# Performance work log

Hardware: AMD Instinct MI355X
Metric: run time of the kernel (lower is better)

## Reference

```python
import jax, jax.numpy as jnp
import numpy as np

# OPT-1.3B attention, decode phase with paged KV cache
E = 2048      # embed_dim
H = 32        # num_heads
D = E // H    # head_dim = 64
S = 64        # num decoding sequences (q_len = 1 each)
L = 2048      # max context length per sequence
BS = 16       # cache block size (vLLM default)
BPS = L // BS # blocks per sequence = 128
NB = S * BPS  # total cache blocks = 8192


def setup_inputs() -> dict:
    key = jax.random.key(0)
    ks = jax.random.split(key, 6)
    hidden_states = jax.random.normal(ks[0], (S, E), jnp.float32) * 0.02
    wqkv = jax.random.normal(ks[1], (E, 3 * E), jnp.float32) * 0.02
    bqkv = jnp.zeros((3 * E,), jnp.float32)
    wout = jax.random.normal(ks[2], (E, E), jnp.float32) * 0.02
    bout = jnp.zeros((E,), jnp.float32)
    key_cache = jax.random.normal(ks[3], (NB, BS, H, D), jnp.float32)
    value_cache = jax.random.normal(ks[4], (NB, BS, H, D), jnp.float32)
    # each sequence owns BPS distinct cache blocks (non-contiguous in general)
    block_tables = jnp.arange(S * BPS, dtype=jnp.int32).reshape(S, BPS)
    context_lens = jax.random.randint(ks[5], (S,), L // 2, L + 1).astype(jnp.int32)
    return dict(hidden_states=hidden_states, wqkv=wqkv, bqkv=bqkv,
                wout=wout, bout=bout, key_cache=key_cache,
                value_cache=value_cache, block_tables=block_tables,
                context_lens=context_lens)


def reference(hidden_states, wqkv, bqkv, wout, bout,
              key_cache, value_cache, block_tables, context_lens):
    scale = 1.0 / np.sqrt(D).astype(np.float32)
    # fused QKV projection
    qkv = hidden_states @ wqkv + bqkv                    # [S, 3E]
    q, k, v = jnp.split(qkv, 3, axis=-1)
    q = q.reshape(S, H, D)
    k_new = k.reshape(S, 1, H, D)
    v_new = v.reshape(S, 1, H, D)
    # paged gather of the KV cache: [S, BPS, BS, H, D] -> [S, L, H, D]
    keys = key_cache[block_tables].reshape(S, L, H, D)
    vals = value_cache[block_tables].reshape(S, L, H, D)
    # decode step attends over cached context plus the current token
    keys = jnp.concatenate([keys, k_new], axis=1)        # [S, L+1, H, D]
    vals = jnp.concatenate([vals, v_new], axis=1)
    scores = jnp.einsum('shd,slhd->shl', q, keys) * scale
    pos = jnp.arange(L + 1)
    valid = (pos[None, :] < context_lens[:, None]) | (pos[None, :] == L)
    scores = jnp.where(valid[:, None, :], scores, jnp.float32(-1e30))
    probs = jax.nn.softmax(scores, axis=-1)              # [S, H, L+1]
    attn = jnp.einsum('shl,slhd->shd', probs, vals).reshape(S, E)
    # output projection
    return attn @ wout + bout
```

## Files before the change

kernel.cpp:

```cpp
#include <hip/hip_runtime.h>
#include <math.h>

#define S_ 64
#define E_ 2048
#define H_ 32
#define D_ 64
#define L_ 2048
#define BS_ 16
#define BPS_ 128
#define QKV_N (3 * E_)
#define CHUNK_CB 8
#define MAXCH 16

__global__ __launch_bounds__(256) void gemm_part(const float* __restrict__ A,
                                                 const float* __restrict__ B,
                                                 float* __restrict__ P,
                                                 int K, int N) {
    __shared__ float As[64][32];
    const int t    = threadIdx.x;
    const int lane = t & 63;
    const int mg   = t >> 6;
    const int colbase = blockIdx.x * 128 + lane * 2;
    const int kchunk  = K / gridDim.y;
    const int ks      = blockIdx.y * kchunk;

    float2 acc[16];
#pragma unroll
    for (int mm = 0; mm < 16; ++mm) acc[mm] = make_float2(0.f, 0.f);

    for (int k0 = ks; k0 < ks + kchunk; k0 += 32) {
        __syncthreads();
#pragma unroll
        for (int i = 0; i < 2; ++i) {
            int f4  = t + i * 256;
            int row = f4 >> 3, c4 = f4 & 7;
            *(float4*)&As[row][c4 * 4] =
                *(const float4*)(A + (size_t)row * K + k0 + c4 * 4);
        }
        __syncthreads();
#pragma unroll
        for (int kk = 0; kk < 32; kk += 4) {
            float2 b0 = *(const float2*)(B + (size_t)(k0 + kk + 0) * N + colbase);
            float2 b1 = *(const float2*)(B + (size_t)(k0 + kk + 1) * N + colbase);
            float2 b2 = *(const float2*)(B + (size_t)(k0 + kk + 2) * N + colbase);
            float2 b3 = *(const float2*)(B + (size_t)(k0 + kk + 3) * N + colbase);
#pragma unroll
            for (int mm = 0; mm < 16; ++mm) {
                float4 a = *(const float4*)&As[mg * 16 + mm][kk];
                acc[mm].x = fmaf(a.x, b0.x, acc[mm].x);
                acc[mm].y = fmaf(a.x, b0.y, acc[mm].y);
                acc[mm].x = fmaf(a.y, b1.x, acc[mm].x);
                acc[mm].y = fmaf(a.y, b1.y, acc[mm].y);
                acc[mm].x = fmaf(a.z, b2.x, acc[mm].x);
                acc[mm].y = fmaf(a.z, b2.y, acc[mm].y);
                acc[mm].x = fmaf(a.w, b3.x, acc[mm].x);
                acc[mm].y = fmaf(a.w, b3.y, acc[mm].y);
            }
        }
    }
    float* Pb = P + (size_t)blockIdx.y * 64 * N;
#pragma unroll
    for (int mm = 0; mm < 16; ++mm)
        *(float2*)(Pb + (size_t)(mg * 16 + mm) * N + colbase) = acc[mm];
}

__global__ __launch_bounds__(256) void reduce_add(const float* __restrict__ P,
                                                  const float* __restrict__ bias,
                                                  float* __restrict__ C,
                                                  int N, int nparts) {
    const int i4     = blockIdx.x * 256 + threadIdx.x;
    const int total4 = 64 * N / 4;
    const int col4   = i4 % (N / 4);
    float4 s = ((const float4*)bias)[col4];
    for (int k = 0; k < nparts; ++k) {
        float4 p = ((const float4*)P)[(size_t)k * total4 + i4];
        s.x += p.x; s.y += p.y; s.z += p.z; s.w += p.w;
    }
    ((float4*)C)[i4] = s;
}

__global__ __launch_bounds__(256, 6) void attn_row(
        const float* __restrict__ qkv,
        const float* __restrict__ kcache,
        const float* __restrict__ vcache,
        const int* __restrict__ btab,
        const int* __restrict__ clens,
        float* __restrict__ ml,
        float* __restrict__ pacc) {
    const int s   = blockIdx.x >> 4;
    const int c   = blockIdx.x & 15;
    const int ctx = clens[s];
    const int nb  = (ctx + 15) >> 4;
    const int cb0 = c * CHUNK_CB;
    if (cb0 >= nb) return;
    const int cb1 = min(cb0 + CHUNK_CB, nb);
    const int t   = threadIdx.x;

    const float* qb = qkv + (size_t)s * QKV_N;
    const float4 q0 = *(const float4*)(qb + t * 4);
    const float4 q1 = *(const float4*)(qb + 1024 + t * 4);

    float m0 = -1e30f, l0 = 0.f, m1 = -1e30f, l1 = 0.f;
    float4 a0 = make_float4(0.f, 0.f, 0.f, 0.f);
    float4 a1 = make_float4(0.f, 0.f, 0.f, 0.f);

    const int* bt = btab + s * BPS_;
    for (int cb = cb0; cb < cb1; ++cb) {
        const int blk = bt[cb];
        const float* kb = kcache + (size_t)blk * (BS_ * H_ * D_);
        const float* vb = vcache + (size_t)blk * (BS_ * H_ * D_);
#pragma unroll 2
        for (int i = 0; i < 16; ++i) {
            const int   tok = cb * 16 + i;
            const int   off = i * 2048 + t * 4;
            const float4 k0 = *(const float4*)(kb + off);
            const float4 k1 = *(const float4*)(kb + off + 1024);
            const float4 v0 = *(const float4*)(vb + off);
            const float4 v1 = *(const float4*)(vb + off + 1024);

            float p0 = q0.x * k0.x + q0.y * k0.y + q0.z * k0.z + q0.w * k0.w;
            float p1 = q1.x * k1.x + q1.y * k1.y + q1.z * k1.z + q1.w * k1.w;
            p0 += __shfl_xor(p0, 1);  p1 += __shfl_xor(p1, 1);
            p0 += __shfl_xor(p0, 2);  p1 += __shfl_xor(p1, 2);
            p0 += __shfl_xor(p0, 4);  p1 += __shfl_xor(p1, 4);
            p0 += __shfl_xor(p0, 8);  p1 += __shfl_xor(p1, 8);

            const bool ok = tok < ctx;
            const float s0 = ok ? p0 * 0.125f : -1e38f;
            const float s1 = ok ? p1 * 0.125f : -1e38f;

            const float nm0 = fmaxf(m0, s0);
            const float r0  = __expf(m0 - nm0);
            const float e0  = __expf(s0 - nm0);
            m0 = nm0;
            l0 = fmaf(l0, r0, e0);
            a0.x = fmaf(e0, v0.x, a0.x * r0);
            a0.y = fmaf(e0, v0.y, a0.y * r0);
            a0.z = fmaf(e0, v0.z, a0.z * r0);
            a0.w = fmaf(e0, v0.w, a0.w * r0);

            const float nm1 = fmaxf(m1, s1);
            const float r1  = __expf(m1 - nm1);
            const float e1  = __expf(s1 - nm1);
            m1 = nm1;
            l1 = fmaf(l1, r1, e1);
            a1.x = fmaf(e1, v1.x, a1.x * r1);
            a1.y = fmaf(e1, v1.y, a1.y * r1);
            a1.z = fmaf(e1, v1.z, a1.z * r1);
            a1.w = fmaf(e1, v1.w, a1.w * r1);
        }
    }

    const int slot = s * MAXCH + c;
    *(float4*)&pacc[(size_t)slot * 2048 + t * 4]        = a0;
    *(float4*)&pacc[(size_t)slot * 2048 + 1024 + t * 4] = a1;
    if ((t & 15) == 0) {
        const int h0 = t >> 4;
        ml[((size_t)slot * 32 + h0) * 2 + 0]        = m0;
        ml[((size_t)slot * 32 + h0) * 2 + 1]        = l0;
        ml[((size_t)slot * 32 + 16 + h0) * 2 + 0]   = m1;
        ml[((size_t)slot * 32 + 16 + h0) * 2 + 1]   = l1;
    }
}

__global__ __launch_bounds__(64) void attn_merge(
        const float* __restrict__ qkv,
        const int* __restrict__ clens,
        const float* __restrict__ ml,
        const float* __restrict__ pacc,
        float* __restrict__ attn) {
    const int sh = blockIdx.x;
    const int s  = sh >> 5;
    const int h  = sh & 31;
    const int d  = threadIdx.x;
    const int ctx = clens[s];
    const int nb  = (ctx + 15) >> 4;
    const int nch = (nb + CHUNK_CB - 1) / CHUNK_CB;

    float M = -1e30f, L = 0.f, O = 0.f;
    for (int c = 0; c < nch; ++c) {
        const int slot = s * MAXCH + c;
        const float mc = ml[((size_t)slot * 32 + h) * 2 + 0];
        const float lc = ml[((size_t)slot * 32 + h) * 2 + 1];
        const float oc = pacc[(size_t)slot * 2048 + h * 64 + d];
        const float nm = fmaxf(M, mc);
        const float ra = __expf(M - nm);
        const float rb = __expf(mc - nm);
        O = O * ra + oc * rb;
        L = L * ra + lc * rb;
        M = nm;
    }

    const float qd = qkv[(size_t)s * QKV_N + h * 64 + d];
    const float kd = qkv[(size_t)s * QKV_N + E_ + h * 64 + d];
    float part = qd * kd;
#pragma unroll
    for (int msk = 1; msk <= 32; msk <<= 1) part += __shfl_xor(part, msk);
    const float score = part * 0.125f;
    const float nm = fmaxf(M, score);
    const float r  = __expf(M - nm);
    const float p  = __expf(score - nm);
    const float vd = qkv[(size_t)s * QKV_N + 2 * E_ + h * 64 + d];
    O = O * r + p * vd;
    L = L * r + p;

    attn[(size_t)s * E_ + h * 64 + d] = O / L;
}

extern "C" void kernel_launch(void* const* d_in, const int* in_sizes, int n_in,
                              void* d_out, int out_size, void* d_ws, size_t ws_size,
                              hipStream_t stream) {
    const float* hidden = (const float*)d_in[0];
    const float* wqkv   = (const float*)d_in[1];
    const float* bqkv   = (const float*)d_in[2];
    const float* wout   = (const float*)d_in[3];
    const float* bout   = (const float*)d_in[4];
    const float* kcache = (const float*)d_in[5];
    const float* vcache = (const float*)d_in[6];
    const int*   btab   = (const int*)d_in[7];
    const int*   clens  = (const int*)d_in[8];
    float* out = (float*)d_out;

    float* qkv     = (float*)d_ws;
    float* attnbuf = qkv + (size_t)S_ * QKV_N;
    float* part1   = attnbuf + (size_t)S_ * E_;
    float* part2   = part1 + (size_t)8 * S_ * QKV_N;
    float* pacc    = part1;
    float* ml      = part2;

    gemm_part<<<dim3(QKV_N / 128, 8), 256, 0, stream>>>(hidden, wqkv, part1,
                                                        E_, QKV_N);
    reduce_add<<<dim3(S_ * QKV_N / 4 / 256), 256, 0, stream>>>(part1, bqkv,
                                                               qkv, QKV_N, 8);
    attn_row<<<dim3(S_ * MAXCH), 256, 0, stream>>>(qkv, kcache, vcache,
                                                   btab, clens, ml, pacc);
    attn_merge<<<dim3(S_ * H_), 64, 0, stream>>>(qkv, clens, ml, pacc, attnbuf);
    gemm_part<<<dim3(E_ / 128, 16), 256, 0, stream>>>(attnbuf, wout, part2,
                                                      E_, E_);
    reduce_add<<<dim3(S_ * E_ / 4 / 256), 256, 0, stream>>>(part2, bout,
                                                            out, E_, 16);
}
```

Before: 387.5 us.

## Fold QKV split-K reduction into attention kernels and use nontemporal KV loads

Removes the separate reduce_add launch for the QKV projection. attn_row and attn_merge now sum the split-K partials plus the bias themselves when they read q/k/v. The QKV GEMM split rises from 8 to 16 K-parts for more parallelism. KV cache loads and partial-accumulator stores switch to nontemporal intrinsics to avoid polluting the cache with streamed data. The trade-off is that each attention block now reads 16 partial rows redundantly; the workspace layout is also rearranged.

```diff
diff --git a/kernel.cpp b/kernel.cpp
--- a/kernel.cpp
+++ b/kernel.cpp
@@ -9,8 +9,20 @@
 #define BS_ 16
 #define BPS_ 128
 #define QKV_N (3 * E_)
+#define KSPL 16
 #define CHUNK_CB 8
 #define MAXCH 16
+
+typedef float f32x4 __attribute__((ext_vector_type(4)));
+
+__device__ __forceinline__ float4 ntload4(const float* p) {
+    f32x4 v = __builtin_nontemporal_load((const f32x4*)p);
+    return make_float4(v.x, v.y, v.z, v.w);
+}
+__device__ __forceinline__ void ntstore4(float* p, float4 v) {
+    f32x4 u = {v.x, v.y, v.z, v.w};
+    __builtin_nontemporal_store(u, (f32x4*)p);
+}
 
 __global__ __launch_bounds__(256) void gemm_part(const float* __restrict__ A,
                                                  const float* __restrict__ B,
@@ -80,7 +92,8 @@
 }
 
 __global__ __launch_bounds__(256, 6) void attn_row(
-        const float* __restrict__ qkv,
+        const float* __restrict__ part1,
+        const float* __restrict__ bqkv,
         const float* __restrict__ kcache,
         const float* __restrict__ vcache,
         const int* __restrict__ btab,
@@ -96,9 +109,16 @@
     const int cb1 = min(cb0 + CHUNK_CB, nb);
     const int t   = threadIdx.x;
 
-    const float* qb = qkv + (size_t)s * QKV_N;
-    const float4 q0 = *(const float4*)(qb + t * 4);
-    const float4 q1 = *(const float4*)(qb + 1024 + t * 4);
+    float4 q0 = *(const float4*)(bqkv + t * 4);
+    float4 q1 = *(const float4*)(bqkv + 1024 + t * 4);
+#pragma unroll 4
+    for (int p = 0; p < KSPL; ++p) {
+        const float* pp = part1 + (size_t)p * S_ * QKV_N + (size_t)s * QKV_N;
+        float4 u0 = *(const float4*)(pp + t * 4);
+        float4 u1 = *(const float4*)(pp + 1024 + t * 4);
+        q0.x += u0.x; q0.y += u0.y; q0.z += u0.z; q0.w += u0.w;
+        q1.x += u1.x; q1.y += u1.y; q1.z += u1.z; q1.w += u1.w;
+    }
 
     float m0 = -1e30f, l0 = 0.f, m1 = -1e30f, l1 = 0.f;
     float4 a0 = make_float4(0.f, 0.f, 0.f, 0.f);
@@ -113,10 +133,10 @@
         for (int i = 0; i < 16; ++i) {
             const int   tok = cb * 16 + i;
             const int   off = i * 2048 + t * 4;
-            const float4 k0 = *(const float4*)(kb + off);
-            const float4 k1 = *(const float4*)(kb + off + 1024);
-            const float4 v0 = *(const float4*)(vb + off);
-            const float4 v1 = *(const float4*)(vb + off + 1024);
+            const float4 k0 = ntload4(kb + off);
+            const float4 k1 = ntload4(kb + off + 1024);
+            const float4 v0 = ntload4(vb + off);
+            const float4 v1 = ntload4(vb + off + 1024);
 
             float p0 = q0.x * k0.x + q0.y * k0.y + q0.z * k0.z + q0.w * k0.w;
             float p1 = q1.x * k1.x + q1.y * k1.y + q1.z * k1.z + q1.w * k1.w;
@@ -152,8 +172,8 @@
     }
 
     const int slot = s * MAXCH + c;
-    *(float4*)&pacc[(size_t)slot * 2048 + t * 4]        = a0;
-    *(float4*)&pacc[(size_t)slot * 2048 + 1024 + t * 4] = a1;
+    ntstore4(&pacc[(size_t)slot * 2048 + t * 4], a0);
+    ntstore4(&pacc[(size_t)slot * 2048 + 1024 + t * 4], a1);
     if ((t & 15) == 0) {
         const int h0 = t >> 4;
         ml[((size_t)slot * 32 + h0) * 2 + 0]        = m0;
@@ -164,7 +184,8 @@
 }
 
 __global__ __launch_bounds__(64) void attn_merge(
-        const float* __restrict__ qkv,
+        const float* __restrict__ part1,
+        const float* __restrict__ bqkv,
         const int* __restrict__ clens,
         const float* __restrict__ ml,
         const float* __restrict__ pacc,
@@ -176,6 +197,16 @@
     const int ctx = clens[s];
     const int nb  = (ctx + 15) >> 4;
     const int nch = (nb + CHUNK_CB - 1) / CHUNK_CB;
+
+    const int col = h * 64 + d;
+    float qd = bqkv[col], kd = bqkv[E_ + col], vd = bqkv[2 * E_ + col];
+#pragma unroll 4
+    for (int p = 0; p < KSPL; ++p) {
+        const float* pp = part1 + (size_t)p * S_ * QKV_N + (size_t)s * QKV_N;
+        qd += pp[col];
+        kd += pp[E_ + col];
+        vd += pp[2 * E_ + col];
+    }
 
     float M = -1e30f, L = 0.f, O = 0.f;
     for (int c = 0; c < nch; ++c) {
@@ -191,8 +222,6 @@
         M = nm;
     }
 
-    const float qd = qkv[(size_t)s * QKV_N + h * 64 + d];
-    const float kd = qkv[(size_t)s * QKV_N + E_ + h * 64 + d];
     float part = qd * kd;
 #pragma unroll
     for (int msk = 1; msk <= 32; msk <<= 1) part += __shfl_xor(part, msk);
@@ -200,7 +229,6 @@
     const float nm = fmaxf(M, score);
     const float r  = __expf(M - nm);
     const float p  = __expf(score - nm);
-    const float vd = qkv[(size_t)s * QKV_N + 2 * E_ + h * 64 + d];
     O = O * r + p * vd;
     L = L * r + p;
 
@@ -221,22 +249,20 @@
     const int*   clens  = (const int*)d_in[8];
     float* out = (float*)d_out;
 
-    float* qkv     = (float*)d_ws;
-    float* attnbuf = qkv + (size_t)S_ * QKV_N;
-    float* part1   = attnbuf + (size_t)S_ * E_;
-    float* part2   = part1 + (size_t)8 * S_ * QKV_N;
-    float* pacc    = part1;
-    float* ml      = part2;
-
-    gemm_part<<<dim3(QKV_N / 128, 8), 256, 0, stream>>>(hidden, wqkv, part1,
-                                                        E_, QKV_N);
-    reduce_add<<<dim3(S_ * QKV_N / 4 / 256), 256, 0, stream>>>(part1, bqkv,
-                                                               qkv, QKV_N, 8);
-    attn_row<<<dim3(S_ * MAXCH), 256, 0, stream>>>(qkv, kcache, vcache,
+    float* part1   = (float*)d_ws;
+    float* attnbuf = part1 + (size_t)KSPL * S_ * QKV_N;
+    float* pacc    = attnbuf + (size_t)S_ * E_;
+    float* ml      = pacc + (size_t)S_ * MAXCH * 2048;
+    float* part2   = pacc;
+
+    gemm_part<<<dim3(QKV_N / 128, KSPL), 256, 0, stream>>>(hidden, wqkv, part1,
+                                                           E_, QKV_N);
+    attn_row<<<dim3(S_ * MAXCH), 256, 0, stream>>>(part1, bqkv, kcache, vcache,
                                                    btab, clens, ml, pacc);
-    attn_merge<<<dim3(S_ * H_), 64, 0, stream>>>(qkv, clens, ml, pacc, attnbuf);
-    gemm_part<<<dim3(E_ / 128, 16), 256, 0, stream>>>(attnbuf, wout, part2,
-                                                      E_, E_);
+    attn_merge<<<dim3(S_ * H_), 64, 0, stream>>>(part1, bqkv, clens, ml, pacc,
+                                                 attnbuf);
+    gemm_part<<<dim3(E_ / 128, KSPL), 256, 0, stream>>>(attnbuf, wout, part2,
+                                                        E_, E_);
     reduce_add<<<dim3(S_ * E_ / 4 / 256), 256, 0, stream>>>(part2, bout,
-                                                            out, E_, 16);
-}
+                                                            out, E_, KSPL);
+}
```

After: 348.3 us. 10.1% less time.
